# Kernel optimization log

Hardware: AMD Instinct MI355X
Metric: run time of the kernel (lower is better)

The kernel has to match this reference:

```python
import jax, jax.numpy as jnp
import numpy as np

N, E, H, L, G = 50000, 500000, 128, 4, 1000
EPS = 1e-7      # GENConv message eps
LN_EPS = 1e-5   # torch LayerNorm default


def setup_inputs() -> dict:
    key = jax.random.key(0)
    ks = jax.random.split(key, 24)
    d = {}
    d["x"] = jax.random.normal(ks[0], (N, 9), jnp.float32)
    d["edge_index"] = jax.random.randint(ks[1], (2, E), 0, N, jnp.int32)
    d["edge_attr"] = jax.random.normal(ks[2], (E, 3), jnp.float32)
    d["batch"] = jnp.sort(jax.random.randint(ks[3], (N,), 0, G, jnp.int32))
    s9, s3, sh, s2h = 1/np.sqrt(9), 1/np.sqrt(3), 1/np.sqrt(H), 1/np.sqrt(2*H)
    u = lambda k, shp, s: jax.random.uniform(k, shp, jnp.float32, -s, s)
    d["enc_node_W"] = u(ks[4], (9, H), s9)
    d["enc_node_b"] = u(ks[5], (H,), s9)
    d["enc_edge_W"] = u(ks[6], (3, H), s3)
    d["enc_edge_b"] = u(ks[7], (H,), s3)
    d["ln_g"] = jnp.ones((L, H), jnp.float32)   # DeepGCNLayer pre-norm affine
    d["ln_b"] = jnp.zeros((L, H), jnp.float32)
    d["W1"] = u(ks[8], (L, H, 2*H), sh)          # GENConv MLP layer 1
    d["b1"] = u(ks[9], (L, 2*H), sh)
    d["mlp_ln_g"] = jnp.ones((L, 2*H), jnp.float32)
    d["mlp_ln_b"] = jnp.zeros((L, 2*H), jnp.float32)
    d["W2"] = u(ks[10], (L, 2*H, H), s2h)        # GENConv MLP layer 2
    d["b2"] = u(ks[11], (L, H), s2h)
    d["t"] = jnp.ones((L,), jnp.float32)         # learnable softmax temperature, init 1.0
    return d


def layernorm(x, g, b):
    mu = x.mean(-1, keepdims=True)
    var = ((x - mu) ** 2).mean(-1, keepdims=True)
    return (x - mu) / jnp.sqrt(var + LN_EPS) * g + b


def genconv(h, src, dst, ea, t, W1, b1, lg, lb, W2, b2):
    # message: relu(x_j + edge_attr) + eps   -> [E, H]
    msg = jax.nn.relu(h[src] + ea) + EPS
    # softmax aggregation over incoming edges, per channel
    logits = t * msg
    m = jax.ops.segment_max(logits, dst, num_segments=N)
    num = jnp.exp(logits - m[dst])
    den = jax.ops.segment_sum(num, dst, num_segments=N)
    alpha = num / den[dst]
    agg = jax.ops.segment_sum(msg * alpha, dst, num_segments=N)
    out = agg + h  # root residual inside GENConv
    z = jax.nn.relu(layernorm(out @ W1 + b1, lg, lb))
    return z @ W2 + b2


def reference(x, edge_index, edge_attr, batch, enc_node_W, enc_node_b,
              enc_edge_W, enc_edge_b, ln_g, ln_b, W1, b1, mlp_ln_g, mlp_ln_b,
              W2, b2, t):
    src, dst = edge_index[0], edge_index[1]
    h = x @ enc_node_W + enc_node_b            # node encoder  [N, H]
    ea = edge_attr @ enc_edge_W + enc_edge_b   # edge encoder  [E, H]
    # layer 0: conv only (DeeperGCN forward uses layers[0].conv directly)
    h = genconv(h, src, dst, ea, t[0], W1[0], b1[0], mlp_ln_g[0], mlp_ln_b[0], W2[0], b2[0])
    # layers 1..L-1: res+ block: x + conv(relu(LN(x))); dropout is identity (eval)
    for i in range(1, L):
        z = jax.nn.relu(layernorm(h, ln_g[i], ln_b[i]))
        h = h + genconv(z, src, dst, ea, t[i], W1[i], b1[i], mlp_ln_g[i], mlp_ln_b[i], W2[i], b2[i])
    h = jax.nn.relu(layernorm(h, ln_g[0], ln_b[0]))  # reuses layer-0 norm
    # global mean pool over graphs
    counts = jax.ops.segment_sum(jnp.ones((N,), h.dtype), batch, num_segments=G)
    sums = jax.ops.segment_sum(h, batch, num_segments=G)
    return sums / jnp.maximum(counts, 1.0)[:, None]
```

## Files before the change

### kernel.cpp

```cpp
#include <hip/hip_runtime.h>

#define NN 50000
#define NE 500000
#define HD 128
#define HD2 256
#define NL 4
#define NG 1000

constexpr float MSG_EPS = 1e-7f;
constexpr float LNEPS   = 1e-5f;

typedef float  f32x4  __attribute__((ext_vector_type(4)));
typedef __bf16 bf16x8 __attribute__((ext_vector_type(8)));

__device__ __forceinline__ unsigned short f2b(float f) {
    unsigned int u = __float_as_uint(f);
    unsigned int r = u + 0x7FFFu + ((u >> 16) & 1u);
    return (unsigned short)(r >> 16);
}
__device__ __forceinline__ float b2f(unsigned short h) {
    return __uint_as_float(((unsigned int)h) << 16);
}

__global__ void k_encode_nodes(const float* __restrict__ x, const float* __restrict__ W,
                               const float* __restrict__ b, unsigned short* __restrict__ zb) {
    int n = blockIdx.x;
    int c = threadIdx.x;
    float xr[9];
#pragma unroll
    for (int k = 0; k < 9; k++) xr[k] = x[n * 9 + k];
    float acc = b[c];
#pragma unroll
    for (int k = 0; k < 9; k++) acc = fmaf(xr[k], W[k * HD + c], acc);
    zb[n * HD + c] = f2b(acc);
}

__global__ void k_prep(const float* __restrict__ W1, const float* __restrict__ W2,
                       unsigned short* __restrict__ W1T, unsigned short* __restrict__ W2T) {
    int idx = blockIdx.x * 256 + threadIdx.x;
    {
        int k = idx & 127, n = (idx >> 7) & 255, l = idx >> 15;
        W1T[idx] = f2b(W1[(l * 128 + k) * 256 + n]);
    }
    {
        int k = idx & 255, n = (idx >> 8) & 127, l = idx >> 15;
        W2T[idx] = f2b(W2[(l * 256 + k) * 128 + n]);
    }
}

__global__ void k_hist(const int* __restrict__ dst, int* __restrict__ counts) {
    int e = blockIdx.x * blockDim.x + threadIdx.x;
    if (e < NE) atomicAdd(&counts[dst[e]], 1);
}

#define SCAN_B 512
__global__ void k_scan1(const int* __restrict__ counts, int* __restrict__ incl,
                        int* __restrict__ bsum) {
    __shared__ int s[SCAN_B];
    int i = blockIdx.x * SCAN_B + threadIdx.x;
    int v = (i < NN) ? counts[i] : 0;
    s[threadIdx.x] = v;
    __syncthreads();
    for (int off = 1; off < SCAN_B; off <<= 1) {
        int t = (threadIdx.x >= off) ? s[threadIdx.x - off] : 0;
        __syncthreads();
        s[threadIdx.x] += t;
        __syncthreads();
    }
    if (i < NN) incl[i] = s[threadIdx.x];
    if (threadIdx.x == SCAN_B - 1) bsum[blockIdx.x] = s[threadIdx.x];
}

__global__ void k_scan2(const int* __restrict__ bsum, int* __restrict__ boff, int nb) {
    __shared__ int s[128];
    int v = (threadIdx.x < nb) ? bsum[threadIdx.x] : 0;
    s[threadIdx.x] = v;
    __syncthreads();
    for (int off = 1; off < 128; off <<= 1) {
        int t = (threadIdx.x >= off) ? s[threadIdx.x - off] : 0;
        __syncthreads();
        s[threadIdx.x] += t;
        __syncthreads();
    }
    if (threadIdx.x < nb) boff[threadIdx.x] = s[threadIdx.x] - v;
}

__global__ void k_scan3(const int* __restrict__ incl, const int* __restrict__ boff,
                        int* __restrict__ row_start) {
    int i = blockIdx.x * SCAN_B + threadIdx.x;
    if (i < NN) row_start[i + 1] = incl[i] + boff[blockIdx.x];
    if (i == 0) row_start[0] = 0;
}

__global__ void k_scatter(const int* __restrict__ src, const int* __restrict__ dst,
                          const float* __restrict__ eattr, const int* __restrict__ row_start,
                          int* __restrict__ cursor, float4* __restrict__ aperm) {
    int e = blockIdx.x * blockDim.x + threadIdx.x;
    if (e >= NE) return;
    int d = dst[e];
    int p = row_start[d] + atomicAdd(&cursor[d], 1);
    float4 v;
    v.x = eattr[e * 3 + 0];
    v.y = eattr[e * 3 + 1];
    v.z = eattr[e * 3 + 2];
    v.w = __int_as_float(src[e]);
    aperm[p] = v;
}

__global__ __launch_bounds__(256) void k_aggregate(const unsigned short* __restrict__ zb,
                                                   const float4* __restrict__ aperm,
                                                   const int* __restrict__ row_start,
                                                   const float* __restrict__ We,
                                                   const float* __restrict__ be,
                                                   const float* __restrict__ t, int layer,
                                                   unsigned int* __restrict__ outb) {
    int w = threadIdx.x >> 6, lane = threadIdx.x & 63;
    int n = blockIdx.x * 4 + w;
    if (n >= NN) return;
    int c = lane * 2;
    float2 w0 = *(const float2*)&We[c];
    float2 w1 = *(const float2*)&We[HD + c];
    float2 w2 = *(const float2*)&We[2 * HD + c];
    float2 bb = *(const float2*)&be[c];
    float tv = t[layer];
    int s0 = row_start[n], s1 = row_start[n + 1];
    float num0 = 0.f, num1 = 0.f, wm0 = 0.f, wm1 = 0.f;
    const unsigned int* z32 = (const unsigned int*)zb;
    int p = s0;
    for (; p + 2 <= s1; p += 2) {
        float4 a0 = aperm[p];
        float4 a1 = aperm[p + 1];
        int sj0 = __float_as_int(a0.w);
        int sj1 = __float_as_int(a1.w);
        unsigned int za = z32[sj0 * 64 + lane];
        unsigned int zc = z32[sj1 * 64 + lane];
        float zax = b2f((unsigned short)za), zay = b2f((unsigned short)(za >> 16));
        float zcx = b2f((unsigned short)zc), zcy = b2f((unsigned short)(zc >> 16));
        float ea0x = fmaf(a0.x, w0.x, fmaf(a0.y, w1.x, fmaf(a0.z, w2.x, bb.x)));
        float ea0y = fmaf(a0.x, w0.y, fmaf(a0.y, w1.y, fmaf(a0.z, w2.y, bb.y)));
        float ea1x = fmaf(a1.x, w0.x, fmaf(a1.y, w1.x, fmaf(a1.z, w2.x, bb.x)));
        float ea1y = fmaf(a1.x, w0.y, fmaf(a1.y, w1.y, fmaf(a1.z, w2.y, bb.y)));
        float m0x = fmaxf(zax + ea0x, 0.f) + MSG_EPS;
        float m0y = fmaxf(zay + ea0y, 0.f) + MSG_EPS;
        float m1x = fmaxf(zcx + ea1x, 0.f) + MSG_EPS;
        float m1y = fmaxf(zcy + ea1y, 0.f) + MSG_EPS;
        float e0x = __expf(tv * m0x), e0y = __expf(tv * m0y);
        float e1x = __expf(tv * m1x), e1y = __expf(tv * m1y);
        num0 += e0x + e1x;
        num1 += e0y + e1y;
        wm0 = fmaf(m0x, e0x, fmaf(m1x, e1x, wm0));
        wm1 = fmaf(m0y, e0y, fmaf(m1y, e1y, wm1));
    }
    if (p < s1) {
        float4 a = aperm[p];
        int sj = __float_as_int(a.w);
        unsigned int za = z32[sj * 64 + lane];
        float zax = b2f((unsigned short)za), zay = b2f((unsigned short)(za >> 16));
        float eax = fmaf(a.x, w0.x, fmaf(a.y, w1.x, fmaf(a.z, w2.x, bb.x)));
        float eay = fmaf(a.x, w0.y, fmaf(a.y, w1.y, fmaf(a.z, w2.y, bb.y)));
        float mx = fmaxf(zax + eax, 0.f) + MSG_EPS;
        float my = fmaxf(zay + eay, 0.f) + MSG_EPS;
        float ex = __expf(tv * mx), ey = __expf(tv * my);
        num0 += ex;
        num1 += ey;
        wm0 = fmaf(mx, ex, wm0);
        wm1 = fmaf(my, ey, wm1);
    }
    unsigned int zn = z32[n * 64 + lane];
    float ox = ((s1 > s0) ? (wm0 / num0) : 0.f) + b2f((unsigned short)zn);
    float oy = ((s1 > s0) ? (wm1 / num1) : 0.f) + b2f((unsigned short)(zn >> 16));
    outb[n * 64 + lane] = (unsigned int)f2b(ox) | ((unsigned int)f2b(oy) << 16);
}

#define HS_LD 268

__global__ __launch_bounds__(64) void k_mlp(const unsigned short* __restrict__ outb,
                                            const unsigned short* __restrict__ W1T,
                                            const float* __restrict__ b1l,
                                            const float* __restrict__ lgl,
                                            const float* __restrict__ lbl,
                                            const unsigned short* __restrict__ W2T,
                                            const float* __restrict__ b2l,
                                            unsigned short* __restrict__ h,
                                            const float* __restrict__ gn,
                                            const float* __restrict__ bn,
                                            unsigned short* __restrict__ zb,
                                            int add_residual) {
    __shared__ __align__(16) unsigned short Hs[16 * HS_LD];

    int base = blockIdx.x * 16;
    int lane = threadIdx.x;
    int q = lane >> 4, i = lane & 15;

    f32x4 acc[16];
#pragma unroll
    for (int ct = 0; ct < 16; ct++) acc[ct] = (f32x4){0.f, 0.f, 0.f, 0.f};

#pragma unroll
    for (int ks = 0; ks < 4; ks++) {
        bf16x8 a = *(const bf16x8*)&outb[(size_t)(base + i) * HD + ks * 32 + q * 8];
#pragma unroll
        for (int ct = 0; ct < 16; ct++) {
            bf16x8 bfr = *(const bf16x8*)&W1T[(ct * 16 + i) * HD + ks * 32 + q * 8];
            acc[ct] = __builtin_amdgcn_mfma_f32_16x16x32_bf16(a, bfr, acc[ct], 0, 0, 0);
        }
    }

#pragma unroll
    for (int ct = 0; ct < 16; ct++) {
        float bb = b1l[ct * 16 + i];
#pragma unroll
        for (int r = 0; r < 4; r++) acc[ct][r] += bb;
    }

    {
        float s[4] = {0.f, 0.f, 0.f, 0.f}, sq[4] = {0.f, 0.f, 0.f, 0.f};
#pragma unroll
        for (int ct = 0; ct < 16; ct++)
#pragma unroll
            for (int r = 0; r < 4; r++) {
                s[r] += acc[ct][r];
                sq[r] = fmaf(acc[ct][r], acc[ct][r], sq[r]);
            }
#pragma unroll
        for (int m = 8; m >= 1; m >>= 1)
#pragma unroll
            for (int r = 0; r < 4; r++) {
                s[r] += __shfl_xor(s[r], m);
                sq[r] += __shfl_xor(sq[r], m);
            }
        float mu[4], inv[4];
#pragma unroll
        for (int r = 0; r < 4; r++) {
            mu[r] = s[r] * (1.f / 256.f);
            float var = sq[r] * (1.f / 256.f) - mu[r] * mu[r];
            inv[r] = rsqrtf(var + LNEPS);
        }
#pragma unroll
        for (int ct = 0; ct < 16; ct++) {
            float g = lgl[ct * 16 + i];
            float c = lbl[ct * 16 + i];
#pragma unroll
            for (int r = 0; r < 4; r++) {
                float v = fmaxf(fmaf((acc[ct][r] - mu[r]) * inv[r], g, c), 0.f);
                Hs[(q * 4 + r) * HS_LD + ct * 16 + i] = f2b(v);
            }
        }
    }

    f32x4 acc2[8];
#pragma unroll
    for (int ct = 0; ct < 8; ct++) acc2[ct] = (f32x4){0.f, 0.f, 0.f, 0.f};

#pragma unroll
    for (int ks = 0; ks < 8; ks++) {
        bf16x8 a = *(const bf16x8*)&Hs[i * HS_LD + ks * 32 + q * 8];
#pragma unroll
        for (int ct = 0; ct < 8; ct++) {
            bf16x8 bfr = *(const bf16x8*)&W2T[(ct * 16 + i) * HD2 + ks * 32 + q * 8];
            acc2[ct] = __builtin_amdgcn_mfma_f32_16x16x32_bf16(a, bfr, acc2[ct], 0, 0, 0);
        }
    }

    if (add_residual) {
#pragma unroll
        for (int ct = 0; ct < 8; ct++) {
            float bb = b2l[ct * 16 + i];
#pragma unroll
            for (int r = 0; r < 4; r++) {
                size_t idx = (size_t)(base + q * 4 + r) * HD + ct * 16 + i;
                acc2[ct][r] += bb + b2f(h[idx]);
            }
        }
    } else {
#pragma unroll
        for (int ct = 0; ct < 8; ct++) {
            float bb = b2l[ct * 16 + i];
#pragma unroll
            for (int r = 0; r < 4; r++) acc2[ct][r] += bb;
        }
    }
#pragma unroll
    for (int ct = 0; ct < 8; ct++)
#pragma unroll
        for (int r = 0; r < 4; r++) {
            size_t idx = (size_t)(base + q * 4 + r) * HD + ct * 16 + i;
            h[idx] = f2b(acc2[ct][r]);
        }

    {
        float s[4] = {0.f, 0.f, 0.f, 0.f}, sq[4] = {0.f, 0.f, 0.f, 0.f};
#pragma unroll
        for (int ct = 0; ct < 8; ct++)
#pragma unroll
            for (int r = 0; r < 4; r++) {
                s[r] += acc2[ct][r];
                sq[r] = fmaf(acc2[ct][r], acc2[ct][r], sq[r]);
            }
#pragma unroll
        for (int m = 8; m >= 1; m >>= 1)
#pragma unroll
            for (int r = 0; r < 4; r++) {
                s[r] += __shfl_xor(s[r], m);
                sq[r] += __shfl_xor(sq[r], m);
            }
        float mu[4], inv[4];
#pragma unroll
        for (int r = 0; r < 4; r++) {
            mu[r] = s[r] * (1.f / 128.f);
            float var = sq[r] * (1.f / 128.f) - mu[r] * mu[r];
            inv[r] = rsqrtf(var + LNEPS);
        }
#pragma unroll
        for (int ct = 0; ct < 8; ct++) {
            float g = gn[ct * 16 + i];
            float c = bn[ct * 16 + i];
#pragma unroll
            for (int r = 0; r < 4; r++) {
                float v = fmaxf(fmaf((acc2[ct][r] - mu[r]) * inv[r], g, c), 0.f);
                zb[(size_t)(base + q * 4 + r) * HD + ct * 16 + i] = f2b(v);
            }
        }
    }
}

__global__ void k_gbounds(const int* __restrict__ batch, int* __restrict__ gstart) {
    int g = blockIdx.x * blockDim.x + threadIdx.x;
    if (g > NG) return;
    int lo = 0, hi = NN;
    while (lo < hi) {
        int mid = (lo + hi) >> 1;
        if (batch[mid] < g) lo = mid + 1;
        else hi = mid;
    }
    gstart[g] = lo;
}

__global__ void k_pool(const unsigned short* __restrict__ zb, const int* __restrict__ gstart,
                       float* __restrict__ out) {
    int g = blockIdx.x;
    int c = threadIdx.x;
    int a = gstart[g], b = gstart[g + 1];
    float s0 = 0.f, s1 = 0.f;
    int n = a;
    for (; n + 2 <= b; n += 2) {
        s0 += b2f(zb[(size_t)n * HD + c]);
        s1 += b2f(zb[(size_t)(n + 1) * HD + c]);
    }
    if (n < b) s0 += b2f(zb[(size_t)n * HD + c]);
    out[g * HD + c] = (s0 + s1) / fmaxf((float)(b - a), 1.f);
}

extern "C" void kernel_launch(void* const* d_in, const int* in_sizes, int n_in, void* d_out,
                              int out_size, void* d_ws, size_t ws_size, hipStream_t stream) {
    const float* x     = (const float*)d_in[0];
    const int* ei      = (const int*)d_in[1];
    const float* eattr = (const float*)d_in[2];
    const int* batch   = (const int*)d_in[3];
    const float* encW  = (const float*)d_in[4];
    const float* encB  = (const float*)d_in[5];
    const float* eW    = (const float*)d_in[6];
    const float* eB    = (const float*)d_in[7];
    const float* ln_g  = (const float*)d_in[8];
    const float* ln_b  = (const float*)d_in[9];
    const float* W1    = (const float*)d_in[10];
    const float* b1    = (const float*)d_in[11];
    const float* mlg   = (const float*)d_in[12];
    const float* mlb   = (const float*)d_in[13];
    const float* W2    = (const float*)d_in[14];
    const float* b2    = (const float*)d_in[15];
    const float* t     = (const float*)d_in[16];
    const int* src = ei;
    const int* dst = ei + NE;

    char* w = (char*)d_ws;
    auto alloc = [&](size_t bytes) {
        char* p = w;
        w += (bytes + 255) & ~size_t(255);
        return p;
    };
    unsigned short* h    = (unsigned short*)alloc(sizeof(unsigned short) * NN * HD);
    unsigned short* zb   = (unsigned short*)alloc(sizeof(unsigned short) * NN * HD);
    unsigned int* outb   = (unsigned int*)alloc(sizeof(unsigned int) * NN * HD / 2);
    float4* aperm        = (float4*)alloc(sizeof(float4) * NE);
    int* row_start       = (int*)alloc(sizeof(int) * (NN + 1));
    int* counts          = (int*)alloc(sizeof(int) * NN);
    int* cursor          = (int*)alloc(sizeof(int) * NN);
    int* incl            = (int*)alloc(sizeof(int) * NN);
    int* bsum            = (int*)alloc(sizeof(int) * 128);
    int* boff            = (int*)alloc(sizeof(int) * 128);
    int* gstart          = (int*)alloc(sizeof(int) * (NG + 1));
    unsigned short* W1T  = (unsigned short*)alloc(sizeof(unsigned short) * NL * HD * HD2);
    unsigned short* W2T  = (unsigned short*)alloc(sizeof(unsigned short) * NL * HD2 * HD);

    hipMemsetAsync(counts, 0, sizeof(int) * NN, stream);
    hipMemsetAsync(cursor, 0, sizeof(int) * NN, stream);

    k_prep<<<512, 256, 0, stream>>>(W1, W2, W1T, W2T);
    k_encode_nodes<<<NN, HD, 0, stream>>>(x, encW, encB, zb);
    k_hist<<<(NE + 255) / 256, 256, 0, stream>>>(dst, counts);
    int nsb = (NN + SCAN_B - 1) / SCAN_B;
    k_scan1<<<nsb, SCAN_B, 0, stream>>>(counts, incl, bsum);
    k_scan2<<<1, 128, 0, stream>>>(bsum, boff, nsb);
    k_scan3<<<nsb, SCAN_B, 0, stream>>>(incl, boff, row_start);
    k_scatter<<<(NE + 255) / 256, 256, 0, stream>>>(src, dst, eattr, row_start, cursor, aperm);
    k_gbounds<<<(NG + 256) / 256, 256, 0, stream>>>(batch, gstart);

    for (int l = 0; l < NL; l++) {
        k_aggregate<<<(NN + 3) / 4, 256, 0, stream>>>(zb, aperm, row_start, eW, eB, t, l, outb);
        int ln_next = (l + 1) % NL;
        k_mlp<<<NN / 16, 64, 0, stream>>>(
            (const unsigned short*)outb, W1T + (size_t)l * HD * HD2, b1 + l * HD2,
            mlg + l * HD2, mlb + l * HD2, W2T + (size_t)l * HD2 * HD, b2 + l * HD, h,
            ln_g + ln_next * HD, ln_b + ln_next * HD, zb, l > 0);
    }
    k_pool<<<NG, HD, 0, stream>>>(zb, gstart, (float*)d_out);
}
```

Measured before the change: 586.1 us.

## Fuse setup kernels, unroll aggregate gathers, widen MLP blocks with staged epilogue

Merges weight prep, node encoding and the degree histogram into one launch, and folds the graph-boundary search into the last scan kernel, cutting launch overhead. The aggregate loop now issues 8 or 4 edge loads and gathers at once, with readfirstlane on the source index, to keep more memory requests in flight. The MLP kernel runs four 16-row waves per block and stages its second GEMM output through shared memory, so the residual add and layernorm work on coalesced row-wise 32-bit accesses with wave-wide shuffles. The cost is more shared memory per block, lower occupancy from larger launch bounds, and more registers in aggregate.

Result: slower. 650.6 us (+11.0%).

```diff
diff --git a/kernel.cpp b/kernel.cpp
--- a/kernel.cpp
+++ b/kernel.cpp
@@ -21,39 +21,49 @@
 __device__ __forceinline__ float b2f(unsigned short h) {
     return __uint_as_float(((unsigned int)h) << 16);
 }
-
-__global__ void k_encode_nodes(const float* __restrict__ x, const float* __restrict__ W,
-                               const float* __restrict__ b, unsigned short* __restrict__ zb) {
-    int n = blockIdx.x;
-    int c = threadIdx.x;
-    float xr[9];
-#pragma unroll
-    for (int k = 0; k < 9; k++) xr[k] = x[n * 9 + k];
-    float acc = b[c];
-#pragma unroll
-    for (int k = 0; k < 9; k++) acc = fmaf(xr[k], W[k * HD + c], acc);
-    zb[n * HD + c] = f2b(acc);
-}
-
-__global__ void k_prep(const float* __restrict__ W1, const float* __restrict__ W2,
-                       unsigned short* __restrict__ W1T, unsigned short* __restrict__ W2T) {
-    int idx = blockIdx.x * 256 + threadIdx.x;
-    {
-        int k = idx & 127, n = (idx >> 7) & 255, l = idx >> 15;
-        W1T[idx] = f2b(W1[(l * 128 + k) * 256 + n]);
-    }
-    {
-        int k = idx & 255, n = (idx >> 8) & 127, l = idx >> 15;
-        W2T[idx] = f2b(W2[(l * 256 + k) * 128 + n]);
-    }
-}
-
-__global__ void k_hist(const int* __restrict__ dst, int* __restrict__ counts) {
-    int e = blockIdx.x * blockDim.x + threadIdx.x;
-    if (e < NE) atomicAdd(&counts[dst[e]], 1);
+__device__ __forceinline__ unsigned int pack2(float a, float b) {
+    return (unsigned int)f2b(a) | ((unsigned int)f2b(b) << 16);
+}
+
+#define PREP_BLKS 512
+#define ENC_BLKS 25000
+#define HIST_BLKS ((NE + 255) / 256)
+
+__global__ void k_setup(const float* __restrict__ x, const float* __restrict__ encW,
+                        const float* __restrict__ encB, unsigned short* __restrict__ zb,
+                        const float* __restrict__ W1, const float* __restrict__ W2,
+                        unsigned short* __restrict__ W1T, unsigned short* __restrict__ W2T,
+                        const int* __restrict__ dst, int* __restrict__ counts) {
+    int bid = blockIdx.x, tid = threadIdx.x;
+    if (bid < PREP_BLKS) {
+        int idx = bid * 256 + tid;
+        {
+            int k = idx & 127, n = (idx >> 7) & 255, l = idx >> 15;
+            W1T[idx] = f2b(W1[(l * 128 + k) * 256 + n]);
+        }
+        {
+            int k = idx & 255, n = (idx >> 8) & 127, l = idx >> 15;
+            W2T[idx] = f2b(W2[(l * 256 + k) * 128 + n]);
+        }
+    } else if (bid < PREP_BLKS + ENC_BLKS) {
+        int n = (bid - PREP_BLKS) * 2 + (tid >> 7);
+        int c = tid & 127;
+        float xr[9];
+#pragma unroll
+        for (int k = 0; k < 9; k++) xr[k] = x[n * 9 + k];
+        float acc = encB[c];
+#pragma unroll
+        for (int k = 0; k < 9; k++) acc = fmaf(xr[k], encW[k * HD + c], acc);
+        zb[(size_t)n * HD + c] = f2b(acc);
+    } else {
+        int e = (bid - PREP_BLKS - ENC_BLKS) * 256 + tid;
+        if (e < NE) atomicAdd(&counts[dst[e]], 1);
+    }
 }
 
 #define SCAN_B 512
+#define NSB ((NN + SCAN_B - 1) / SCAN_B)
+
 __global__ void k_scan1(const int* __restrict__ counts, int* __restrict__ incl,
                         int* __restrict__ bsum) {
     __shared__ int s[SCAN_B];
@@ -85,11 +95,24 @@
     if (threadIdx.x < nb) boff[threadIdx.x] = s[threadIdx.x] - v;
 }
 
-__global__ void k_scan3(const int* __restrict__ incl, const int* __restrict__ boff,
-                        int* __restrict__ row_start) {
-    int i = blockIdx.x * SCAN_B + threadIdx.x;
-    if (i < NN) row_start[i + 1] = incl[i] + boff[blockIdx.x];
-    if (i == 0) row_start[0] = 0;
+__global__ void k_scan3g(const int* __restrict__ incl, const int* __restrict__ boff,
+                         int* __restrict__ row_start, const int* __restrict__ batch,
+                         int* __restrict__ gstart) {
+    if (blockIdx.x < NSB) {
+        int i = blockIdx.x * SCAN_B + threadIdx.x;
+        if (i < NN) row_start[i + 1] = incl[i] + boff[blockIdx.x];
+        if (i == 0) row_start[0] = 0;
+    } else {
+        int g = (blockIdx.x - NSB) * SCAN_B + threadIdx.x;
+        if (g > NG) return;
+        int lo = 0, hi = NN;
+        while (lo < hi) {
+            int mid = (lo + hi) >> 1;
+            if (batch[mid] < g) lo = mid + 1;
+            else hi = mid;
+        }
+        gstart[g] = lo;
+    }
 }
 
 __global__ void k_scatter(const int* __restrict__ src, const int* __restrict__ dst,
@@ -107,7 +130,22 @@
     aperm[p] = v;
 }
 
-__global__ __launch_bounds__(256) void k_aggregate(const unsigned short* __restrict__ zb,
+__device__ __forceinline__ void edge_acc2(float4 a, unsigned int zz, float2 w0, float2 w1,
+                                          float2 w2, float2 bb, float tv, float& num0,
+                                          float& num1, float& wm0, float& wm1) {
+    float zx = b2f((unsigned short)zz), zy = b2f((unsigned short)(zz >> 16));
+    float eax = fmaf(a.x, w0.x, fmaf(a.y, w1.x, fmaf(a.z, w2.x, bb.x)));
+    float eay = fmaf(a.x, w0.y, fmaf(a.y, w1.y, fmaf(a.z, w2.y, bb.y)));
+    float mx = fmaxf(zx + eax, 0.f) + MSG_EPS;
+    float my = fmaxf(zy + eay, 0.f) + MSG_EPS;
+    float ex = __expf(tv * mx), ey = __expf(tv * my);
+    num0 += ex;
+    num1 += ey;
+    wm0 = fmaf(mx, ex, wm0);
+    wm1 = fmaf(my, ey, wm1);
+}
+
+__global__ __launch_bounds__(256) void k_aggregate(const unsigned short* __restrict__ zbin,
                                                    const float4* __restrict__ aperm,
                                                    const int* __restrict__ row_start,
                                                    const float* __restrict__ We,
@@ -125,77 +163,76 @@
     float tv = t[layer];
     int s0 = row_start[n], s1 = row_start[n + 1];
     float num0 = 0.f, num1 = 0.f, wm0 = 0.f, wm1 = 0.f;
-    const unsigned int* z32 = (const unsigned int*)zb;
+    const unsigned int* z32 = (const unsigned int*)zbin;
     int p = s0;
-    for (; p + 2 <= s1; p += 2) {
-        float4 a0 = aperm[p];
-        float4 a1 = aperm[p + 1];
-        int sj0 = __float_as_int(a0.w);
-        int sj1 = __float_as_int(a1.w);
-        unsigned int za = z32[sj0 * 64 + lane];
-        unsigned int zc = z32[sj1 * 64 + lane];
-        float zax = b2f((unsigned short)za), zay = b2f((unsigned short)(za >> 16));
-        float zcx = b2f((unsigned short)zc), zcy = b2f((unsigned short)(zc >> 16));
-        float ea0x = fmaf(a0.x, w0.x, fmaf(a0.y, w1.x, fmaf(a0.z, w2.x, bb.x)));
-        float ea0y = fmaf(a0.x, w0.y, fmaf(a0.y, w1.y, fmaf(a0.z, w2.y, bb.y)));
-        float ea1x = fmaf(a1.x, w0.x, fmaf(a1.y, w1.x, fmaf(a1.z, w2.x, bb.x)));
-        float ea1y = fmaf(a1.x, w0.y, fmaf(a1.y, w1.y, fmaf(a1.z, w2.y, bb.y)));
-        float m0x = fmaxf(zax + ea0x, 0.f) + MSG_EPS;
-        float m0y = fmaxf(zay + ea0y, 0.f) + MSG_EPS;
-        float m1x = fmaxf(zcx + ea1x, 0.f) + MSG_EPS;
-        float m1y = fmaxf(zcy + ea1y, 0.f) + MSG_EPS;
-        float e0x = __expf(tv * m0x), e0y = __expf(tv * m0y);
-        float e1x = __expf(tv * m1x), e1y = __expf(tv * m1y);
-        num0 += e0x + e1x;
-        num1 += e0y + e1y;
-        wm0 = fmaf(m0x, e0x, fmaf(m1x, e1x, wm0));
-        wm1 = fmaf(m0y, e0y, fmaf(m1y, e1y, wm1));
-    }
-    if (p < s1) {
+    for (; p + 8 <= s1; p += 8) {
+        float4 A[8];
+#pragma unroll
+        for (int j = 0; j < 8; j++) A[j] = aperm[p + j];
+        unsigned int Z[8];
+#pragma unroll
+        for (int j = 0; j < 8; j++) {
+            int sj = __builtin_amdgcn_readfirstlane(__float_as_int(A[j].w));
+            Z[j] = z32[(size_t)sj * 64 + lane];
+        }
+#pragma unroll
+        for (int j = 0; j < 8; j++)
+            edge_acc2(A[j], Z[j], w0, w1, w2, bb, tv, num0, num1, wm0, wm1);
+    }
+    for (; p + 4 <= s1; p += 4) {
+        float4 A[4];
+#pragma unroll
+        for (int j = 0; j < 4; j++) A[j] = aperm[p + j];
+        unsigned int Z[4];
+#pragma unroll
+        for (int j = 0; j < 4; j++) {
+            int sj = __builtin_amdgcn_readfirstlane(__float_as_int(A[j].w));
+            Z[j] = z32[(size_t)sj * 64 + lane];
+        }
+#pragma unroll
+        for (int j = 0; j < 4; j++)
+            edge_acc2(A[j], Z[j], w0, w1, w2, bb, tv, num0, num1, wm0, wm1);
+    }
+    for (; p < s1; p++) {
         float4 a = aperm[p];
-        int sj = __float_as_int(a.w);
-        unsigned int za = z32[sj * 64 + lane];
-        float zax = b2f((unsigned short)za), zay = b2f((unsigned short)(za >> 16));
-        float eax = fmaf(a.x, w0.x, fmaf(a.y, w1.x, fmaf(a.z, w2.x, bb.x)));
-        float eay = fmaf(a.x, w0.y, fmaf(a.y, w1.y, fmaf(a.z, w2.y, bb.y)));
-        float mx = fmaxf(zax + eax, 0.f) + MSG_EPS;
-        float my = fmaxf(zay + eay, 0.f) + MSG_EPS;
-        float ex = __expf(tv * mx), ey = __expf(tv * my);
-        num0 += ex;
-        num1 += ey;
-        wm0 = fmaf(mx, ex, wm0);
-        wm1 = fmaf(my, ey, wm1);
-    }
-    unsigned int zn = z32[n * 64 + lane];
+        int sj = __builtin_amdgcn_readfirstlane(__float_as_int(a.w));
+        unsigned int zz = z32[(size_t)sj * 64 + lane];
+        edge_acc2(a, zz, w0, w1, w2, bb, tv, num0, num1, wm0, wm1);
+    }
+    unsigned int zn = z32[(size_t)n * 64 + lane];
     float ox = ((s1 > s0) ? (wm0 / num0) : 0.f) + b2f((unsigned short)zn);
     float oy = ((s1 > s0) ? (wm1 / num1) : 0.f) + b2f((unsigned short)(zn >> 16));
-    outb[n * 64 + lane] = (unsigned int)f2b(ox) | ((unsigned int)f2b(oy) << 16);
+    outb[(size_t)n * 64 + lane] = pack2(ox, oy);
 }
 
 #define HS_LD 268
-
-__global__ __launch_bounds__(64) void k_mlp(const unsigned short* __restrict__ outb,
-                                            const unsigned short* __restrict__ W1T,
-                                            const float* __restrict__ b1l,
-                                            const float* __restrict__ lgl,
-                                            const float* __restrict__ lbl,
-                                            const unsigned short* __restrict__ W2T,
-                                            const float* __restrict__ b2l,
-                                            unsigned short* __restrict__ h,
-                                            const float* __restrict__ gn,
-                                            const float* __restrict__ bn,
-                                            unsigned short* __restrict__ zb,
-                                            int add_residual) {
-    __shared__ __align__(16) unsigned short Hs[16 * HS_LD];
-
-    int base = blockIdx.x * 16;
-    int lane = threadIdx.x;
-    int q = lane >> 4, i = lane & 15;
+#define HT_LD 136
+
+__global__ __launch_bounds__(256) void k_mlp(const unsigned short* __restrict__ outb,
+                                             const unsigned short* __restrict__ W1T,
+                                             const float* __restrict__ b1l,
+                                             const float* __restrict__ lgl,
+                                             const float* __restrict__ lbl,
+                                             const unsigned short* __restrict__ W2T,
+                                             const float* __restrict__ b2l,
+                                             unsigned short* __restrict__ h,
+                                             const float* __restrict__ gn,
+                                             const float* __restrict__ bn,
+                                             unsigned short* __restrict__ zb,
+                                             int add_residual) {
+    __shared__ __align__(16) unsigned short Hs[4 * 16 * HS_LD];
+    __shared__ __align__(16) unsigned short Ht[4 * 16 * HT_LD];
+
+    int tid = threadIdx.x;
+    int w = tid >> 6, lane = tid & 63, q = lane >> 4, i = lane & 15;
+    int base = blockIdx.x * 64 + w * 16;
+    if (base >= NN) return;
+    unsigned short* hs = Hs + w * 16 * HS_LD;
+    unsigned short* ht = Ht + w * 16 * HT_LD;
 
     f32x4 acc[16];
 #pragma unroll
     for (int ct = 0; ct < 16; ct++) acc[ct] = (f32x4){0.f, 0.f, 0.f, 0.f};
-
 #pragma unroll
     for (int ks = 0; ks < 4; ks++) {
         bf16x8 a = *(const bf16x8*)&outb[(size_t)(base + i) * HD + ks * 32 + q * 8];
@@ -205,7 +242,6 @@
             acc[ct] = __builtin_amdgcn_mfma_f32_16x16x32_bf16(a, bfr, acc[ct], 0, 0, 0);
         }
     }
-
 #pragma unroll
     for (int ct = 0; ct < 16; ct++) {
         float bb = b1l[ct * 16 + i];
@@ -239,11 +275,11 @@
 #pragma unroll
         for (int ct = 0; ct < 16; ct++) {
             float g = lgl[ct * 16 + i];
-            float c = lbl[ct * 16 + i];
+            float cb = lbl[ct * 16 + i];
 #pragma unroll
             for (int r = 0; r < 4; r++) {
-                float v = fmaxf(fmaf((acc[ct][r] - mu[r]) * inv[r], g, c), 0.f);
-                Hs[(q * 4 + r) * HS_LD + ct * 16 + i] = f2b(v);
+                float v = fmaxf(fmaf((acc[ct][r] - mu[r]) * inv[r], g, cb), 0.f);
+                hs[(q * 4 + r) * HS_LD + ct * 16 + i] = f2b(v);
             }
         }
     }
@@ -251,10 +287,9 @@
     f32x4 acc2[8];
 #pragma unroll
     for (int ct = 0; ct < 8; ct++) acc2[ct] = (f32x4){0.f, 0.f, 0.f, 0.f};
-
 #pragma unroll
     for (int ks = 0; ks < 8; ks++) {
-        bf16x8 a = *(const bf16x8*)&Hs[i * HS_LD + ks * 32 + q * 8];
+        bf16x8 a = *(const bf16x8*)&hs[i * HS_LD + ks * 32 + q * 8];
 #pragma unroll
         for (int ct = 0; ct < 8; ct++) {
             bf16x8 bfr = *(const bf16x8*)&W2T[(ct * 16 + i) * HD2 + ks * 32 + q * 8];
@@ -262,78 +297,44 @@
         }
     }
 
-    if (add_residual) {
-#pragma unroll
-        for (int ct = 0; ct < 8; ct++) {
-            float bb = b2l[ct * 16 + i];
-#pragma unroll
-            for (int r = 0; r < 4; r++) {
-                size_t idx = (size_t)(base + q * 4 + r) * HD + ct * 16 + i;
-                acc2[ct][r] += bb + b2f(h[idx]);
+#pragma unroll
+    for (int ct = 0; ct < 8; ct++) {
+        float bb = b2l[ct * 16 + i];
+#pragma unroll
+        for (int r = 0; r < 4; r++)
+            ht[(q * 4 + r) * HT_LD + ct * 16 + i] = f2b(acc2[ct][r] + bb);
+    }
+
+    {
+        const unsigned int* ht32 = (const unsigned int*)ht;
+        unsigned int* h32 = (unsigned int*)h;
+        unsigned int* zb32 = (unsigned int*)zb;
+        float2 gg = *(const float2*)&gn[lane * 2];
+        float2 cc = *(const float2*)&bn[lane * 2];
+        for (int rr = 0; rr < 16; rr++) {
+            int row = base + rr;
+            unsigned int tv = ht32[rr * (HT_LD / 2) + lane];
+            float cx = b2f((unsigned short)tv), cy = b2f((unsigned short)(tv >> 16));
+            if (add_residual) {
+                unsigned int hv = h32[(size_t)row * 64 + lane];
+                cx += b2f((unsigned short)hv);
+                cy += b2f((unsigned short)(hv >> 16));
             }
-        }
-    } else {
-#pragma unroll
-        for (int ct = 0; ct < 8; ct++) {
-            float bb = b2l[ct * 16 + i];
-#pragma unroll
-            for (int r = 0; r < 4; r++) acc2[ct][r] += bb;
-        }
-    }
-#pragma unroll
-    for (int ct = 0; ct < 8; ct++)
-#pragma unroll
-        for (int r = 0; r < 4; r++) {
-            size_t idx = (size_t)(base + q * 4 + r) * HD + ct * 16 + i;
-            h[idx] = f2b(acc2[ct][r]);
-        }
-
-    {
-        float s[4] = {0.f, 0.f, 0.f, 0.f}, sq[4] = {0.f, 0.f, 0.f, 0.f};
-#pragma unroll
-        for (int ct = 0; ct < 8; ct++)
-#pragma unroll
-            for (int r = 0; r < 4; r++) {
-                s[r] += acc2[ct][r];
-                sq[r] = fmaf(acc2[ct][r], acc2[ct][r], sq[r]);
+            h32[(size_t)row * 64 + lane] = pack2(cx, cy);
+            float s = cx + cy, sq = cx * cx + cy * cy;
+#pragma unroll
+            for (int m = 32; m >= 1; m >>= 1) {
+                s += __shfl_xor(s, m);
+                sq += __shfl_xor(sq, m);
             }
-#pragma unroll
-        for (int m = 8; m >= 1; m >>= 1)
-#pragma unroll
-            for (int r = 0; r < 4; r++) {
-                s[r] += __shfl_xor(s[r], m);
-                sq[r] += __shfl_xor(sq[r], m);
-            }
-        float mu[4], inv[4];
-#pragma unroll
-        for (int r = 0; r < 4; r++) {
-            mu[r] = s[r] * (1.f / 128.f);
-            float var = sq[r] * (1.f / 128.f) - mu[r] * mu[r];
-            inv[r] = rsqrtf(var + LNEPS);
-        }
-#pragma unroll
-        for (int ct = 0; ct < 8; ct++) {
-            float g = gn[ct * 16 + i];
-            float c = bn[ct * 16 + i];
-#pragma unroll
-            for (int r = 0; r < 4; r++) {
-                float v = fmaxf(fmaf((acc2[ct][r] - mu[r]) * inv[r], g, c), 0.f);
-                zb[(size_t)(base + q * 4 + r) * HD + ct * 16 + i] = f2b(v);
-            }
-        }
-    }
-}
-
-__global__ void k_gbounds(const int* __restrict__ batch, int* __restrict__ gstart) {
-    int g = blockIdx.x * blockDim.x + threadIdx.x;
-    if (g > NG) return;
-    int lo = 0, hi = NN;
-    while (lo < hi) {
-        int mid = (lo + hi) >> 1;
-        if (batch[mid] < g) lo = mid + 1;
-        else hi = mid;
-    }
-    gstart[g] = lo;
+            float mu = s * (1.f / 128.f);
+            float var = sq * (1.f / 128.f) - mu * mu;
+            float inv = rsqrtf(var + LNEPS);
+            float z0 = fmaxf(fmaf((cx - mu) * inv, gg.x, cc.x), 0.f);
+            float z1 = fmaxf(fmaf((cy - mu) * inv, gg.y, cc.y), 0.f);
+            zb32[(size_t)row * 64 + lane] = pack2(z0, z1);
+        }
+    }
 }
 
 __global__ void k_pool(const unsigned short* __restrict__ zb, const int* __restrict__ gstart,
@@ -396,20 +397,17 @@
     hipMemsetAsync(counts, 0, sizeof(int) * NN, stream);
     hipMemsetAsync(cursor, 0, sizeof(int) * NN, stream);
 
-    k_prep<<<512, 256, 0, stream>>>(W1, W2, W1T, W2T);
-    k_encode_nodes<<<NN, HD, 0, stream>>>(x, encW, encB, zb);
-    k_hist<<<(NE + 255) / 256, 256, 0, stream>>>(dst, counts);
-    int nsb = (NN + SCAN_B - 1) / SCAN_B;
-    k_scan1<<<nsb, SCAN_B, 0, stream>>>(counts, incl, bsum);
-    k_scan2<<<1, 128, 0, stream>>>(bsum, boff, nsb);
-    k_scan3<<<nsb, SCAN_B, 0, stream>>>(incl, boff, row_start);
+    k_setup<<<PREP_BLKS + ENC_BLKS + HIST_BLKS, 256, 0, stream>>>(x, encW, encB, zb, W1, W2,
+                                                                  W1T, W2T, dst, counts);
+    k_scan1<<<NSB, SCAN_B, 0, stream>>>(counts, incl, bsum);
+    k_scan2<<<1, 128, 0, stream>>>(bsum, boff, NSB);
+    k_scan3g<<<NSB + 2, SCAN_B, 0, stream>>>(incl, boff, row_start, batch, gstart);
     k_scatter<<<(NE + 255) / 256, 256, 0, stream>>>(src, dst, eattr, row_start, cursor, aperm);
-    k_gbounds<<<(NG + 256) / 256, 256, 0, stream>>>(batch, gstart);
 
     for (int l = 0; l < NL; l++) {
         k_aggregate<<<(NN + 3) / 4, 256, 0, stream>>>(zb, aperm, row_start, eW, eB, t, l, outb);
         int ln_next = (l + 1) % NL;
-        k_mlp<<<NN / 16, 64, 0, stream>>>(
+        k_mlp<<<(NN + 63) / 64, 256, 0, stream>>>(
             (const unsigned short*)outb, W1T + (size_t)l * HD * HD2, b1 + l * HD2,
             mlg + l * HD2, mlb + l * HD2, W2T + (size_t)l * HD2 * HD, b2 + l * HD, h,
             ln_g + ln_next * HD, ln_b + ln_next * HD, zb, l > 0);
```
